# Kernel tuning notes

Measured on AMD Instinct MI355X. Metric: run time of the kernel, lower is better.

Reference implementation:

```python
import jax, jax.numpy as jnp
import numpy as np

B, S, H, NH, L, MLP_MULT = 4, 1024, 1024, 16, 2, 4
DK = H // NH
EPS = 1e-5


def setup_inputs() -> dict:
    key = jax.random.key(0)
    ks = jax.random.split(key, 8)
    p = lambda k, shape: jax.random.normal(k, shape, dtype=jnp.float32) * 0.02
    return {
        'hidden_states': jax.random.normal(ks[0], (B, S, H), dtype=jnp.float32),
        'attn_w': p(ks[1], (L, H, 3 * H)),
        'attn_b': jnp.zeros((L, 3 * H), jnp.float32),
        'proj_w': p(ks[2], (L, H, H)),
        'proj_b': jnp.zeros((L, H), jnp.float32),
        'fc_w': p(ks[3], (L, H, MLP_MULT * H)),
        'fc_b': jnp.zeros((L, MLP_MULT * H), jnp.float32),
        'fc2_w': p(ks[4], (L, MLP_MULT * H, H)),
        'fc2_b': jnp.zeros((L, H), jnp.float32),
        'ln1_g': jnp.ones((L, H), jnp.float32),
        'ln1_b': jnp.zeros((L, H), jnp.float32),
        'ln2_g': jnp.ones((L, H), jnp.float32),
        'ln2_b': jnp.zeros((L, H), jnp.float32),
        'position_ids': jnp.arange(S, dtype=jnp.int32),
    }


def _ln(x, g, b):
    m = jnp.mean(x, axis=-1, keepdims=True)
    v = jnp.var(x, axis=-1, keepdims=True)
    return (x - m) * jax.lax.rsqrt(v + EPS) * g + b


def _rotate_half(x):
    x1, x2 = jnp.split(x, 2, axis=-1)
    return jnp.concatenate((-x2, x1), axis=-1)


def _forward(hidden_states, attn_w, attn_b, proj_w, proj_b, fc_w, fc_b,
             fc2_w, fc2_b, ln1_g, ln1_b, ln2_g, ln2_b, position_ids):
    # rotary tables (fp32 math, as in RotaryEmbedding.forward)
    inv_freq = 1.0 / (10000.0 ** (jnp.arange(0, DK, 2, dtype=jnp.float32) / DK))
    freqs = position_ids.astype(jnp.float32)[:, None] * inv_freq[None, :]  # [S, DK/2]
    emb = jnp.concatenate((freqs, freqs), axis=-1)                          # [S, DK]
    cos = jnp.cos(emb)[None, None]  # [1,1,S,DK]
    sin = jnp.sin(emb)[None, None]
    causal = jnp.tril(jnp.ones((S, S), dtype=bool))
    neg = jnp.finfo(jnp.float32).min
    scale = 1.0 / np.sqrt(DK).astype(np.float32)

    h = hidden_states
    for i in range(L):
        # attention block
        x = _ln(h, ln1_g[i], ln1_b[i])
        qkv = x @ attn_w[i] + attn_b[i]                  # Conv1D c_attn
        q, k, v = jnp.split(qkv, 3, axis=-1)
        heads = lambda t: t.reshape(B, S, NH, DK).transpose(0, 2, 1, 3)
        q, k, v = heads(q), heads(k), heads(v)           # [B,NH,S,DK]
        q = q * cos + _rotate_half(q) * sin
        k = k * cos + _rotate_half(k) * sin
        # fp32 QK^T (baddbmm with alpha=scale, beta=0)
        w = jnp.einsum('bhqd,bhkd->bhqk', q.astype(jnp.float32),
                       k.astype(jnp.float32)) * scale    # [B,NH,S,S]
        w = jnp.where(causal, w, neg)
        w = jax.nn.softmax(w, axis=-1).astype(v.dtype)   # attn dropout is identity (eval)
        a = jnp.einsum('bhqk,bhkd->bhqd', w, v)
        a = a.transpose(0, 2, 1, 3).reshape(B, S, H)     # merge_heads
        h = h + (a @ proj_w[i] + proj_b[i])              # c_proj + residual
        # MLP block (gelu_new == tanh-approx gelu)
        x = _ln(h, ln2_g[i], ln2_b[i])
        mid = jax.nn.gelu(x @ fc_w[i] + fc_b[i], approximate=True)
        h = h + (mid @ fc2_w[i] + fc2_b[i])
    return h


def reference(hidden_states, attn_w, attn_b, proj_w, proj_b, fc_w, fc_b,
              fc2_w, fc2_b, ln1_g, ln1_b, ln2_g, ln2_b, position_ids):
    return _forward(hidden_states, attn_w, attn_b, proj_w, proj_b, fc_w, fc_b,
                    fc2_w, fc2_b, ln1_g, ln1_b, ln2_g, ln2_b, position_ids)
```

## Files before the change

### kernel.cpp

```cpp
#include <hip/hip_runtime.h>

#define B_ 4
#define S_ 1024
#define H_ 1024
#define NH_ 16
#define DK_ 64
#define MLPH_ 4096
#define EPS_ 1e-5f

typedef __attribute__((ext_vector_type(8))) short short8_t;
typedef __attribute__((ext_vector_type(8))) unsigned short ushort8_t;
typedef __attribute__((ext_vector_type(4))) float f32x4;

__device__ __forceinline__ unsigned short f2bf(float f) {
  unsigned int u = __float_as_uint(f);
  u = u + 0x7fffu + ((u >> 16) & 1u);
  return (unsigned short)(u >> 16);
}
__device__ __forceinline__ float bf2f(unsigned short b) {
  return __uint_as_float(((unsigned int)b) << 16);
}

__device__ __forceinline__ void gload16(const void* g, void* l) {
  typedef const __attribute__((address_space(1))) unsigned int GU;
  typedef __attribute__((address_space(3))) unsigned int LU;
  __builtin_amdgcn_global_load_lds((GU*)(size_t)g, (LU*)(unsigned int)(size_t)l, 16, 0, 0);
}

__device__ __forceinline__ float gelu_tanh(float x) {
  float y = 1.5957691216057308f * (x + 0.044715f * x * x * x);
  return x / (1.0f + __expf(-y));
}

__global__ __launch_bounds__(256) void wconv(const float* __restrict__ src,
                                             unsigned short* __restrict__ dst,
                                             int K, int N) {
  __shared__ float t[32][33];
  int n0 = blockIdx.x * 32, k0 = blockIdx.y * 32;
  int tid = threadIdx.x;
  int r = tid >> 3, c = (tid & 7) * 4;
  const float* s = src + (size_t)(k0 + r) * N + n0 + c;
  float4 v = *(const float4*)s;
  t[r][c] = v.x; t[r][c + 1] = v.y; t[r][c + 2] = v.z; t[r][c + 3] = v.w;
  __syncthreads();
  ushort4 o;
  o.x = f2bf(t[c + 0][r]); o.y = f2bf(t[c + 1][r]);
  o.z = f2bf(t[c + 2][r]); o.w = f2bf(t[c + 3][r]);
  *(ushort4*)(dst + (size_t)(n0 + r) * K + k0 + c) = o;
}

__global__ __launch_bounds__(256) void ln_kernel(const float* __restrict__ x,
                                                 const float* __restrict__ g,
                                                 const float* __restrict__ b,
                                                 unsigned short* __restrict__ y) {
  int row = blockIdx.x, tid = threadIdx.x;
  const float* xp = x + (size_t)row * H_;
  float4 v = *((const float4*)xp + tid);
  float s  = v.x + v.y + v.z + v.w;
  float s2 = v.x * v.x + v.y * v.y + v.z * v.z + v.w * v.w;
  #pragma unroll
  for (int o = 1; o < 64; o <<= 1) {
    s  += __shfl_xor(s, o, 64);
    s2 += __shfl_xor(s2, o, 64);
  }
  __shared__ float r1[4], r2[4];
  if ((tid & 63) == 0) { r1[tid >> 6] = s; r2[tid >> 6] = s2; }
  __syncthreads();
  s  = r1[0] + r1[1] + r1[2] + r1[3];
  s2 = r2[0] + r2[1] + r2[2] + r2[3];
  float mean = s * (1.0f / H_);
  float var  = s2 * (1.0f / H_) - mean * mean;
  float inv  = rsqrtf(var + EPS_);
  float4 gv = *((const float4*)g + tid);
  float4 bv = *((const float4*)b + tid);
  ushort4 o;
  o.x = f2bf((v.x - mean) * inv * gv.x + bv.x);
  o.y = f2bf((v.y - mean) * inv * gv.y + bv.y);
  o.z = f2bf((v.z - mean) * inv * gv.z + bv.z);
  o.w = f2bf((v.w - mean) * inv * gv.w + bv.w);
  *(ushort4*)(y + (size_t)row * H_ + tid * 4) = o;
}

__global__ __launch_bounds__(256) void rope_bf(unsigned short* qkv, const int* __restrict__ pos) {
  int idx = blockIdx.x * 256 + threadIdx.x;
  int d = idx & 31;
  int hh = (idx >> 5) & 15;
  int s = (idx >> 9) & 1023;
  int b = idx >> 19;
  size_t base = ((size_t)(b * S_ + s)) * 3072 + hh * 64;
  float inv = __expf(-9.210340371976184f * ((float)d * 0.03125f));
  float th = (float)pos[s] * inv;
  float cs = cosf(th), sn = sinf(th);
  unsigned short* qp = qkv + base;
  unsigned short* kp = qkv + base + 1024;
  float q0 = bf2f(qp[d]), q1 = bf2f(qp[d + 32]);
  float k0 = bf2f(kp[d]), k1 = bf2f(kp[d + 32]);
  qp[d]      = f2bf(q0 * cs - q1 * sn);
  qp[d + 32] = f2bf(q1 * cs + q0 * sn);
  kp[d]      = f2bf(k0 * cs - k1 * sn);
  kp[d + 32] = f2bf(k1 * cs + k0 * sn);
}

template <int MODE, int NT>
__global__ __launch_bounds__(256) void gemm_mfma(
    const unsigned short* __restrict__ A, const unsigned short* __restrict__ Bt,
    const float* __restrict__ bias, const float* __restrict__ resid,
    void* __restrict__ outp, int M, int N, int K) {
  constexpr int BN = NT * 32;
  constexpr int CB = BN / 32;
  __shared__ __align__(16) unsigned short As[2][128 * 64];
  __shared__ __align__(16) unsigned short Bs[2][BN * 64];
  int tid = threadIdx.x;
  int w = tid >> 6, lane = tid & 63;
  int gx = gridDim.x;
  int nwg = gx * gridDim.y;
  int bid = blockIdx.y * gx + blockIdx.x;
  int cpx = nwg >> 3;
  int swz = (bid & 7) * cpx + (bid >> 3);
  int m0 = (swz / gx) * 128, n0 = (swz % gx) * BN;
  int wr = w >> 1, wc = w & 1;
  int fr = lane & 15, kg = lane >> 4;
  f32x4 acc[4][NT];
  #pragma unroll
  for (int m = 0; m < 4; m++)
    #pragma unroll
    for (int n = 0; n < NT; n++) {
      acc[m][n][0] = 0.f; acc[m][n][1] = 0.f; acc[m][n][2] = 0.f; acc[m][n][3] = 0.f;
    }
  int srow = lane >> 3;
  int scol = ((lane & 7) ^ srow) * 8;
  const unsigned short* Ap = A  + (size_t)(m0 + w * 32 + srow) * K + scol;
  const unsigned short* Bp = Bt + (size_t)(n0 + w * (8 * CB) + srow) * K + scol;
  int sx = (fr & 7);
  int nk = K >> 6;
  {
    char* AsB = (char*)As[0] + w * 4096;
    char* BsB = (char*)Bs[0] + w * CB * 1024;
    #pragma unroll
    for (int i = 0; i < 4; i++) gload16(Ap + (size_t)i * 8 * K, AsB + i * 1024);
    #pragma unroll
    for (int i = 0; i < CB; i++) gload16(Bp + (size_t)i * 8 * K, BsB + i * 1024);
  }
  __syncthreads();
  for (int t = 0; t < nk; t++) {
    int cur = t & 1;
    if (t + 1 < nk) {
      const unsigned short* Ap2 = Ap + (size_t)(t + 1) * 64;
      const unsigned short* Bp2 = Bp + (size_t)(t + 1) * 64;
      char* AsB = (char*)As[cur ^ 1] + w * 4096;
      char* BsB = (char*)Bs[cur ^ 1] + w * CB * 1024;
      #pragma unroll
      for (int i = 0; i < 4; i++) gload16(Ap2 + (size_t)i * 8 * K, AsB + i * 1024);
      #pragma unroll
      for (int i = 0; i < CB; i++) gload16(Bp2 + (size_t)i * 8 * K, BsB + i * 1024);
    }
    #pragma unroll
    for (int kk = 0; kk < 2; kk++) {
      int slot = ((kk * 4 + kg) ^ sx) << 4;
      short8_t af[4], bfr[NT];
      #pragma unroll
      for (int m = 0; m < 4; m++)
        af[m] = *(const short8_t*)((char*)As[cur] + (wr * 64 + m * 16 + fr) * 128 + slot);
      #pragma unroll
      for (int n = 0; n < NT; n++)
        bfr[n] = *(const short8_t*)((char*)Bs[cur] + (wc * (NT * 16) + n * 16 + fr) * 128 + slot);
      #pragma unroll
      for (int m = 0; m < 4; m++)
        #pragma unroll
        for (int n = 0; n < NT; n++)
          acc[m][n] = __builtin_amdgcn_mfma_f32_16x16x32_bf16(af[m], bfr[n], acc[m][n], 0, 0, 0);
    }
    __syncthreads();
  }
  #pragma unroll
  for (int n = 0; n < NT; n++) {
    int col = n0 + wc * (NT * 16) + n * 16 + fr;
    float bv = bias[col];
    #pragma unroll
    for (int m = 0; m < 4; m++) {
      int row = m0 + wr * 64 + m * 16 + kg * 4;
      #pragma unroll
      for (int r = 0; r < 4; r++) {
        float v = acc[m][n][r] + bv;
        size_t idx = (size_t)(row + r) * N + col;
        if (MODE == 2)      ((float*)outp)[idx] = resid[idx] + v;
        else if (MODE == 1) ((unsigned short*)outp)[idx] = f2bf(gelu_tanh(v));
        else                ((unsigned short*)outp)[idx] = f2bf(v);
      }
    }
  }
}

__global__ __launch_bounds__(256) void attn5(const unsigned short* __restrict__ qkv,
                                             unsigned short* __restrict__ aout) {
  __shared__ __align__(16) unsigned short Ks[2][64 * 64];
  __shared__ __align__(16) unsigned short Vt[2][64 * 64];
  __shared__ __align__(16) unsigned short Ps[4][2][16 * 64];
  int tid = threadIdx.x;
  int w = tid >> 6, lane = tid & 63;
  int fr = lane & 15, kg = lane >> 4;
  int qt = (int)gridDim.x - 1 - (int)blockIdx.x;
  int q0 = qt * 128;
  int head = blockIdx.y, b = blockIdx.z;
  const unsigned short* base = qkv + ((size_t)b * S_) * 3072 + head * 64;

  short8_t qa0[2], qa1[2];
  #pragma unroll
  for (int g = 0; g < 2; g++) {
    const unsigned short* qp = base + (size_t)(q0 + w * 32 + g * 16 + fr) * 3072 + kg * 8;
    qa0[g] = *(const short8_t*)qp;
    qa1[g] = *(const short8_t*)(qp + 32);
  }

  f32x4 acc[2][4];
  float mrun[2][4], lrun[2][4];
  #pragma unroll
  for (int g = 0; g < 2; g++)
    #pragma unroll
    for (int n = 0; n < 4; n++) {
      acc[g][n][0] = 0.f; acc[g][n][1] = 0.f; acc[g][n][2] = 0.f; acc[g][n][3] = 0.f;
      mrun[g][n] = -3.0e38f; lrun[g][n] = 0.f;
    }

  int skv = lane;
  int sd0 = w * 16;

  const unsigned short* kp0 = base + 1024 + (size_t)skv * 3072 + sd0;
  short8_t ka = *(const short8_t*)kp0;
  short8_t kb = *(const short8_t*)(kp0 + 8);
  short8_t va = *(const short8_t*)(kp0 + 1024);
  short8_t vb = *(const short8_t*)(kp0 + 1032);

  int ntiles = 2 * qt + 2;
  for (int t = 0; t < ntiles; t++) {
    int cur = t & 1;
    {
      unsigned kbyte = skv * 128 + sd0 * 2;
      unsigned ksw = (skv & 7) << 4;
      *(short8_t*)((char*)Ks[cur] + (kbyte ^ ksw)) = ka;
      *(short8_t*)((char*)Ks[cur] + ((kbyte + 16) ^ ksw)) = kb;
      #pragma unroll
      for (int j = 0; j < 8; j++) {
        int d0 = sd0 + j, d1 = sd0 + 8 + j;
        *(unsigned short*)((char*)Vt[cur] + ((d0 * 128 + skv * 2) ^ ((d0 & 7) << 4))) = (unsigned short)va[j];
        *(unsigned short*)((char*)Vt[cur] + ((d1 * 128 + skv * 2) ^ ((d1 & 7) << 4))) = (unsigned short)vb[j];
      }
    }
    if (t + 1 < ntiles) {
      const unsigned short* kp = base + 1024 + (size_t)((t + 1) * 64 + skv) * 3072 + sd0;
      ka = *(const short8_t*)kp;
      kb = *(const short8_t*)(kp + 8);
      va = *(const short8_t*)(kp + 1024);
      vb = *(const short8_t*)(kp + 1032);
    }
    __syncthreads();
    f32x4 s[2][4];
    {
      short8_t b0[4], b1[4];
      #pragma unroll
      for (int n = 0; n < 4; n++) {
        int kvrow = n * 16 + fr;
        unsigned sw = (kvrow & 7) << 4;
        b0[n] = *(const short8_t*)((char*)Ks[cur] + ((kvrow * 128 + kg * 16) ^ sw));
        b1[n] = *(const short8_t*)((char*)Ks[cur] + ((kvrow * 128 + 64 + kg * 16) ^ sw));
      }
      __builtin_amdgcn_s_setprio(1);
      #pragma unroll
      for (int g = 0; g < 2; g++)
        #pragma unroll
        for (int n = 0; n < 4; n++) {
          f32x4 z; z[0] = 0.f; z[1] = 0.f; z[2] = 0.f; z[3] = 0.f;
          z = __builtin_amdgcn_mfma_f32_16x16x32_bf16(qa0[g], b0[n], z, 0, 0, 0);
          z = __builtin_amdgcn_mfma_f32_16x16x32_bf16(qa1[g], b1[n], z, 0, 0, 0);
          s[g][n] = z;
        }
      __builtin_amdgcn_s_setprio(0);
    }
    bool diag = (t >= 2 * qt);
    float pmax[2][4];
    #pragma unroll
    for (int g = 0; g < 2; g++)
      #pragma unroll
      for (int r = 0; r < 4; r++) {
        int qrow = q0 + w * 32 + g * 16 + kg * 4 + r;
        float rm = -3.0e38f;
        #pragma unroll
        for (int n = 0; n < 4; n++) {
          float sv = s[g][n][r] * 0.125f;
          if (diag && (t * 64 + n * 16 + fr > qrow)) sv = -3.0e38f;
          s[g][n][r] = sv;
          rm = fmaxf(rm, sv);
        }
        pmax[g][r] = rm;
      }
    bool need = false;
    #pragma unroll
    for (int g = 0; g < 2; g++)
      #pragma unroll
      for (int r = 0; r < 4; r++) need |= (pmax[g][r] > mrun[g][r] + 8.f);
    if (__any(need)) {
      #pragma unroll
      for (int g = 0; g < 2; g++)
        #pragma unroll
        for (int r = 0; r < 4; r++) {
          float rm = pmax[g][r];
          rm = fmaxf(rm, __shfl_xor(rm, 1, 64));
          rm = fmaxf(rm, __shfl_xor(rm, 2, 64));
          rm = fmaxf(rm, __shfl_xor(rm, 4, 64));
          rm = fmaxf(rm, __shfl_xor(rm, 8, 64));
          float mn = fmaxf(mrun[g][r], rm);
          float sc = __expf(mrun[g][r] - mn);
          mrun[g][r] = mn;
          lrun[g][r] *= sc;
          #pragma unroll
          for (int n = 0; n < 4; n++) acc[g][n][r] *= sc;
        }
    }
    #pragma unroll
    for (int g = 0; g < 2; g++)
      #pragma unroll
      for (int r = 0; r < 4; r++) {
        float ls = 0.f;
        int row = kg * 4 + r;
        #pragma unroll
        for (int n = 0; n < 4; n++) {
          float e = __expf(s[g][n][r] - mrun[g][r]);
          ls += e;
          int col = n * 16 + fr;
          *(unsigned short*)((char*)Ps[w][g] + ((row * 128 + col * 2) ^ ((row & 7) << 4))) = f2bf(e);
        }
        lrun[g][r] += ls;
      }
    asm volatile("s_waitcnt lgkmcnt(0)" ::: "memory");
    unsigned psw = (fr & 7) << 4;
    short8_t pa0[2], pa1[2];
    #pragma unroll
    for (int g = 0; g < 2; g++) {
      pa0[g] = *(const short8_t*)((char*)Ps[w][g] + ((fr * 128 + kg * 16) ^ psw));
      pa1[g] = *(const short8_t*)((char*)Ps[w][g] + ((fr * 128 + 64 + kg * 16) ^ psw));
    }
    __builtin_amdgcn_s_setprio(1);
    #pragma unroll
    for (int n = 0; n < 4; n++) {
      int d = n * 16 + fr;
      unsigned sw = (d & 7) << 4;
      short8_t v0 = *(const short8_t*)((char*)Vt[cur] + ((d * 128 + kg * 16) ^ sw));
      short8_t v1 = *(const short8_t*)((char*)Vt[cur] + ((d * 128 + 64 + kg * 16) ^ sw));
      #pragma unroll
      for (int g = 0; g < 2; g++) {
        acc[g][n] = __builtin_amdgcn_mfma_f32_16x16x32_bf16(pa0[g], v0, acc[g][n], 0, 0, 0);
        acc[g][n] = __builtin_amdgcn_mfma_f32_16x16x32_bf16(pa1[g], v1, acc[g][n], 0, 0, 0);
      }
    }
    __builtin_amdgcn_s_setprio(0);
  }
  #pragma unroll
  for (int g = 0; g < 2; g++)
    #pragma unroll
    for (int r = 0; r < 4; r++) {
      float ls = lrun[g][r];
      ls += __shfl_xor(ls, 1, 64);
      ls += __shfl_xor(ls, 2, 64);
      ls += __shfl_xor(ls, 4, 64);
      ls += __shfl_xor(ls, 8, 64);
      float inv = 1.0f / ls;
      size_t row = (size_t)b * S_ + q0 + w * 32 + g * 16 + kg * 4 + r;
      unsigned short* op = aout + row * H_ + head * 64 + fr;
      #pragma unroll
      for (int n = 0; n < 4; n++) op[n * 16] = f2bf(acc[g][n][r] * inv);
    }
}

extern "C" void kernel_launch(void* const* d_in, const int* in_sizes, int n_in,
                              void* d_out, int out_size, void* d_ws, size_t ws_size,
                              hipStream_t stream) {
  const float* hs     = (const float*)d_in[0];
  const float* attn_w = (const float*)d_in[1];
  const float* attn_b = (const float*)d_in[2];
  const float* proj_w = (const float*)d_in[3];
  const float* proj_b = (const float*)d_in[4];
  const float* fc_w   = (const float*)d_in[5];
  const float* fc_b   = (const float*)d_in[6];
  const float* fc2_w  = (const float*)d_in[7];
  const float* fc2_b  = (const float*)d_in[8];
  const float* ln1_g  = (const float*)d_in[9];
  const float* ln1_b  = (const float*)d_in[10];
  const float* ln2_g  = (const float*)d_in[11];
  const float* ln2_b  = (const float*)d_in[12];
  const int*   pos    = (const int*)d_in[13];

  float* hres = (float*)d_out;
  const size_t rows = (size_t)B_ * S_;

  unsigned short* wQ    = (unsigned short*)d_ws;
  unsigned short* wP    = wQ  + (size_t)2 * 3072 * 1024;
  unsigned short* wF1   = wP  + (size_t)2 * 1024 * 1024;
  unsigned short* wF2   = wF1 + (size_t)2 * 4096 * 1024;
  unsigned short* xbf   = wF2 + (size_t)2 * 1024 * 4096;
  unsigned short* qkvbf = xbf + rows * H_;
  unsigned short* midbf = qkvbf + rows * 3 * H_;
  unsigned short* aoutbf= midbf + rows * MLPH_;

  hipMemcpyAsync(hres, hs, rows * H_ * sizeof(float), hipMemcpyDeviceToDevice, stream);

  for (int l = 0; l < 2; l++) {
    wconv<<<dim3(96, 32), 256, 0, stream>>>(attn_w + (size_t)l * 1024 * 3072,
                                            wQ + (size_t)l * 3072 * 1024, 1024, 3072);
    wconv<<<dim3(32, 32), 256, 0, stream>>>(proj_w + (size_t)l * 1024 * 1024,
                                            wP + (size_t)l * 1024 * 1024, 1024, 1024);
    wconv<<<dim3(128, 32), 256, 0, stream>>>(fc_w + (size_t)l * 1024 * 4096,
                                             wF1 + (size_t)l * 4096 * 1024, 1024, 4096);
    wconv<<<dim3(32, 128), 256, 0, stream>>>(fc2_w + (size_t)l * 4096 * 1024,
                                             wF2 + (size_t)l * 1024 * 4096, 4096, 1024);
  }

  for (int l = 0; l < 2; l++) {
    ln_kernel<<<rows, 256, 0, stream>>>(hres, ln1_g + l * H_, ln1_b + l * H_, xbf);
    gemm_mfma<0, 4><<<dim3(24, 32), 256, 0, stream>>>(
        xbf, wQ + (size_t)l * 3072 * 1024, attn_b + (size_t)l * 3072, nullptr,
        qkvbf, 4096, 3072, 1024);
    rope_bf<<<8192, 256, 0, stream>>>(qkvbf, pos);
    attn5<<<dim3(8, 16, 4), 256, 0, stream>>>(qkvbf, aoutbf);
    gemm_mfma<2, 2><<<dim3(16, 32), 256, 0, stream>>>(
        aoutbf, wP + (size_t)l * 1024 * 1024, proj_b + (size_t)l * 1024, hres,
        hres, 4096, 1024, 1024);
    ln_kernel<<<rows, 256, 0, stream>>>(hres, ln2_g + l * H_, ln2_b + l * H_, xbf);
    gemm_mfma<1, 4><<<dim3(32, 32), 256, 0, stream>>>(
        xbf, wF1 + (size_t)l * 4096 * 1024, fc_b + (size_t)l * 4096, nullptr,
        midbf, 4096, 4096, 1024);
    gemm_mfma<2, 2><<<dim3(16, 32), 256, 0, stream>>>(
        midbf, wF2 + (size_t)l * 1024 * 4096, fc2_b + (size_t)l * 1024, hres,
        hres, 4096, 1024, 4096);
  }
}
```

Measured before the change: 466.2 us.

## Fuse RoPE into QKV GEMM epilogue, transpose attention MFMA layout, batch weight conversion

The separate rope_bf kernel is removed and rotary embedding is applied in a new MODE 3 epilogue of the QKV GEMM, using the fact that each 128-column tile holds both halves of a head. The attention kernel now computes S^T and O^T by swapping the MFMA operands, so each lane owns one query row: softmax max and sum reductions need only two shuffles, exp2 replaces exp with a pre-folded log2e scale, P is packed with v_cvt_pk_bf16_f32, and output stores are vectorized. Weight-conversion launches are merged across layers with a z grid dimension. This removes a full read-modify-write pass over Q and K and cuts per-row reduction work, at the cost of more epilogue complexity and sincos inside the GEMM.

```diff
diff --git a/kernel.cpp b/kernel.cpp
--- a/kernel.cpp
+++ b/kernel.cpp
@@ -32,10 +32,12 @@
   return x / (1.0f + __expf(-y));
 }
 
-__global__ __launch_bounds__(256) void wconv(const float* __restrict__ src,
-                                             unsigned short* __restrict__ dst,
+__global__ __launch_bounds__(256) void wconv(const float* __restrict__ src0,
+                                             unsigned short* __restrict__ dst0,
                                              int K, int N) {
   __shared__ float t[32][33];
+  const float* src = src0 + (size_t)blockIdx.z * K * N;
+  unsigned short* dst = dst0 + (size_t)blockIdx.z * N * K;
   int n0 = blockIdx.x * 32, k0 = blockIdx.y * 32;
   int tid = threadIdx.x;
   int r = tid >> 3, c = (tid & 7) * 4;
@@ -81,31 +83,11 @@
   *(ushort4*)(y + (size_t)row * H_ + tid * 4) = o;
 }
 
-__global__ __launch_bounds__(256) void rope_bf(unsigned short* qkv, const int* __restrict__ pos) {
-  int idx = blockIdx.x * 256 + threadIdx.x;
-  int d = idx & 31;
-  int hh = (idx >> 5) & 15;
-  int s = (idx >> 9) & 1023;
-  int b = idx >> 19;
-  size_t base = ((size_t)(b * S_ + s)) * 3072 + hh * 64;
-  float inv = __expf(-9.210340371976184f * ((float)d * 0.03125f));
-  float th = (float)pos[s] * inv;
-  float cs = cosf(th), sn = sinf(th);
-  unsigned short* qp = qkv + base;
-  unsigned short* kp = qkv + base + 1024;
-  float q0 = bf2f(qp[d]), q1 = bf2f(qp[d + 32]);
-  float k0 = bf2f(kp[d]), k1 = bf2f(kp[d + 32]);
-  qp[d]      = f2bf(q0 * cs - q1 * sn);
-  qp[d + 32] = f2bf(q1 * cs + q0 * sn);
-  kp[d]      = f2bf(k0 * cs - k1 * sn);
-  kp[d + 32] = f2bf(k1 * cs + k0 * sn);
-}
-
 template <int MODE, int NT>
 __global__ __launch_bounds__(256) void gemm_mfma(
     const unsigned short* __restrict__ A, const unsigned short* __restrict__ Bt,
     const float* __restrict__ bias, const float* __restrict__ resid,
-    void* __restrict__ outp, int M, int N, int K) {
+    void* __restrict__ outp, int M, int N, int K, const int* __restrict__ pos) {
   constexpr int BN = NT * 32;
   constexpr int CB = BN / 32;
   __shared__ __align__(16) unsigned short As[2][128 * 64];
@@ -172,6 +154,48 @@
     }
     __syncthreads();
   }
+  if (MODE == 3) {
+    int seg = n0 >> 10;
+    if (seg < 2) {
+      #pragma unroll
+      for (int n = 0; n < 2; n++) {
+        int col0 = n0 + wc * 64 + n * 16 + fr;
+        int d2 = n * 16 + fr;
+        float invf = __expf(-0.2878231366242557f * (float)d2);
+        float bv0 = bias[col0], bv2 = bias[col0 + 32];
+        #pragma unroll
+        for (int m = 0; m < 4; m++) {
+          int row = m0 + wr * 64 + m * 16 + kg * 4;
+          #pragma unroll
+          for (int r = 0; r < 4; r++) {
+            int s = (row + r) & (S_ - 1);
+            float th = (float)pos[s] * invf;
+            float sn, cs;
+            __sincosf(th, &sn, &cs);
+            float a0 = acc[m][n][r] + bv0;
+            float a2 = acc[m][n + 2][r] + bv2;
+            size_t base = (size_t)(row + r) * N;
+            ((unsigned short*)outp)[base + col0]      = f2bf(a0 * cs - a2 * sn);
+            ((unsigned short*)outp)[base + col0 + 32] = f2bf(a2 * cs + a0 * sn);
+          }
+        }
+      }
+    } else {
+      #pragma unroll
+      for (int n = 0; n < NT; n++) {
+        int col = n0 + wc * (NT * 16) + n * 16 + fr;
+        float bv = bias[col];
+        #pragma unroll
+        for (int m = 0; m < 4; m++) {
+          int row = m0 + wr * 64 + m * 16 + kg * 4;
+          #pragma unroll
+          for (int r = 0; r < 4; r++)
+            ((unsigned short*)outp)[(size_t)(row + r) * N + col] = f2bf(acc[m][n][r] + bv);
+        }
+      }
+    }
+    return;
+  }
   #pragma unroll
   for (int n = 0; n < NT; n++) {
     int col = n0 + wc * (NT * 16) + n * 16 + fr;
@@ -191,11 +215,13 @@
   }
 }
 
-__global__ __launch_bounds__(256) void attn5(const unsigned short* __restrict__ qkv,
+__global__ __launch_bounds__(256) void attn6(const unsigned short* __restrict__ qkv,
                                              unsigned short* __restrict__ aout) {
   __shared__ __align__(16) unsigned short Ks[2][64 * 64];
   __shared__ __align__(16) unsigned short Vt[2][64 * 64];
   __shared__ __align__(16) unsigned short Ps[4][2][16 * 64];
+  const float SCL2 = 0.18033688011112443f;
+  const float THR2 = 11.541560327111708f;
   int tid = threadIdx.x;
   int w = tid >> 6, lane = tid & 63;
   int fr = lane & 15, kg = lane >> 4;
@@ -213,17 +239,21 @@
   }
 
   f32x4 acc[2][4];
-  float mrun[2][4], lrun[2][4];
-  #pragma unroll
-  for (int g = 0; g < 2; g++)
+  float mrun[2], lrun[2];
+  #pragma unroll
+  for (int g = 0; g < 2; g++) {
+    mrun[g] = -3.0e38f; lrun[g] = 0.f;
     #pragma unroll
     for (int n = 0; n < 4; n++) {
       acc[g][n][0] = 0.f; acc[g][n][1] = 0.f; acc[g][n][2] = 0.f; acc[g][n][3] = 0.f;
-      mrun[g][n] = -3.0e38f; lrun[g][n] = 0.f;
-    }
+    }
+  }
 
   int skv = lane;
   int sd0 = w * 16;
+  int qg[2];
+  qg[0] = q0 + w * 32 + fr;
+  qg[1] = qg[0] + 16;
 
   const unsigned short* kp0 = base + 1024 + (size_t)skv * 3072 + sd0;
   short8_t ka = *(const short8_t*)kp0;
@@ -254,7 +284,7 @@
       vb = *(const short8_t*)(kp + 1032);
     }
     __syncthreads();
-    f32x4 s[2][4];
+    f32x4 st[2][4];
     {
       short8_t b0[4], b1[4];
       #pragma unroll
@@ -270,67 +300,63 @@
         #pragma unroll
         for (int n = 0; n < 4; n++) {
           f32x4 z; z[0] = 0.f; z[1] = 0.f; z[2] = 0.f; z[3] = 0.f;
-          z = __builtin_amdgcn_mfma_f32_16x16x32_bf16(qa0[g], b0[n], z, 0, 0, 0);
-          z = __builtin_amdgcn_mfma_f32_16x16x32_bf16(qa1[g], b1[n], z, 0, 0, 0);
-          s[g][n] = z;
+          z = __builtin_amdgcn_mfma_f32_16x16x32_bf16(b0[n], qa0[g], z, 0, 0, 0);
+          z = __builtin_amdgcn_mfma_f32_16x16x32_bf16(b1[n], qa1[g], z, 0, 0, 0);
+          st[g][n] = z;
         }
       __builtin_amdgcn_s_setprio(0);
     }
     bool diag = (t >= 2 * qt);
-    float pmax[2][4];
-    #pragma unroll
-    for (int g = 0; g < 2; g++)
-      #pragma unroll
-      for (int r = 0; r < 4; r++) {
-        int qrow = q0 + w * 32 + g * 16 + kg * 4 + r;
-        float rm = -3.0e38f;
-        #pragma unroll
-        for (int n = 0; n < 4; n++) {
-          float sv = s[g][n][r] * 0.125f;
-          if (diag && (t * 64 + n * 16 + fr > qrow)) sv = -3.0e38f;
-          s[g][n][r] = sv;
+    float pmax[2];
+    #pragma unroll
+    for (int g = 0; g < 2; g++) {
+      float rm = -3.0e38f;
+      #pragma unroll
+      for (int n = 0; n < 4; n++)
+        #pragma unroll
+        for (int j = 0; j < 4; j++) {
+          float sv = st[g][n][j] * SCL2;
+          if (diag && (t * 64 + n * 16 + kg * 4 + j > qg[g])) sv = -1.0e30f;
+          st[g][n][j] = sv;
           rm = fmaxf(rm, sv);
         }
-        pmax[g][r] = rm;
-      }
-    bool need = false;
-    #pragma unroll
-    for (int g = 0; g < 2; g++)
-      #pragma unroll
-      for (int r = 0; r < 4; r++) need |= (pmax[g][r] > mrun[g][r] + 8.f);
+      pmax[g] = rm;
+    }
+    bool need = (pmax[0] > mrun[0] + THR2) | (pmax[1] > mrun[1] + THR2);
     if (__any(need)) {
       #pragma unroll
-      for (int g = 0; g < 2; g++)
-        #pragma unroll
-        for (int r = 0; r < 4; r++) {
-          float rm = pmax[g][r];
-          rm = fmaxf(rm, __shfl_xor(rm, 1, 64));
-          rm = fmaxf(rm, __shfl_xor(rm, 2, 64));
-          rm = fmaxf(rm, __shfl_xor(rm, 4, 64));
-          rm = fmaxf(rm, __shfl_xor(rm, 8, 64));
-          float mn = fmaxf(mrun[g][r], rm);
-          float sc = __expf(mrun[g][r] - mn);
-          mrun[g][r] = mn;
-          lrun[g][r] *= sc;
-          #pragma unroll
-          for (int n = 0; n < 4; n++) acc[g][n][r] *= sc;
+      for (int g = 0; g < 2; g++) {
+        float rm = pmax[g];
+        rm = fmaxf(rm, __shfl_xor(rm, 16, 64));
+        rm = fmaxf(rm, __shfl_xor(rm, 32, 64));
+        float mn = fmaxf(mrun[g], rm);
+        float sc = exp2f(mrun[g] - mn);
+        mrun[g] = mn;
+        lrun[g] *= sc;
+        #pragma unroll
+        for (int n = 0; n < 4; n++) {
+          acc[g][n][0] *= sc; acc[g][n][1] *= sc; acc[g][n][2] *= sc; acc[g][n][3] *= sc;
         }
-    }
-    #pragma unroll
-    for (int g = 0; g < 2; g++)
-      #pragma unroll
-      for (int r = 0; r < 4; r++) {
-        float ls = 0.f;
-        int row = kg * 4 + r;
-        #pragma unroll
-        for (int n = 0; n < 4; n++) {
-          float e = __expf(s[g][n][r] - mrun[g][r]);
-          ls += e;
-          int col = n * 16 + fr;
-          *(unsigned short*)((char*)Ps[w][g] + ((row * 128 + col * 2) ^ ((row & 7) << 4))) = f2bf(e);
-        }
-        lrun[g][r] += ls;
-      }
+      }
+    }
+    #pragma unroll
+    for (int g = 0; g < 2; g++) {
+      float ls = 0.f;
+      #pragma unroll
+      for (int n = 0; n < 4; n++) {
+        float e0 = exp2f(st[g][n][0] - mrun[g]);
+        float e1 = exp2f(st[g][n][1] - mrun[g]);
+        float e2 = exp2f(st[g][n][2] - mrun[g]);
+        float e3 = exp2f(st[g][n][3] - mrun[g]);
+        ls += (e0 + e1) + (e2 + e3);
+        unsigned lo, hi;
+        asm("v_cvt_pk_bf16_f32 %0, %1, %2" : "=v"(lo) : "v"(e0), "v"(e1));
+        asm("v_cvt_pk_bf16_f32 %0, %1, %2" : "=v"(hi) : "v"(e2), "v"(e3));
+        uint2 pk; pk.x = lo; pk.y = hi;
+        *(uint2*)((char*)Ps[w][g] + ((fr * 128 + n * 32 + kg * 8) ^ ((fr & 7) << 4))) = pk;
+      }
+      lrun[g] += ls;
+    }
     asm volatile("s_waitcnt lgkmcnt(0)" ::: "memory");
     unsigned psw = (fr & 7) << 4;
     short8_t pa0[2], pa1[2];
@@ -348,27 +374,30 @@
       short8_t v1 = *(const short8_t*)((char*)Vt[cur] + ((d * 128 + 64 + kg * 16) ^ sw));
       #pragma unroll
       for (int g = 0; g < 2; g++) {
-        acc[g][n] = __builtin_amdgcn_mfma_f32_16x16x32_bf16(pa0[g], v0, acc[g][n], 0, 0, 0);
-        acc[g][n] = __builtin_amdgcn_mfma_f32_16x16x32_bf16(pa1[g], v1, acc[g][n], 0, 0, 0);
+        acc[g][n] = __builtin_amdgcn_mfma_f32_16x16x32_bf16(v0, pa0[g], acc[g][n], 0, 0, 0);
+        acc[g][n] = __builtin_amdgcn_mfma_f32_16x16x32_bf16(v1, pa1[g], acc[g][n], 0, 0, 0);
       }
     }
     __builtin_amdgcn_s_setprio(0);
   }
   #pragma unroll
-  for (int g = 0; g < 2; g++)
-    #pragma unroll
-    for (int r = 0; r < 4; r++) {
-      float ls = lrun[g][r];
-      ls += __shfl_xor(ls, 1, 64);
-      ls += __shfl_xor(ls, 2, 64);
-      ls += __shfl_xor(ls, 4, 64);
-      ls += __shfl_xor(ls, 8, 64);
-      float inv = 1.0f / ls;
-      size_t row = (size_t)b * S_ + q0 + w * 32 + g * 16 + kg * 4 + r;
-      unsigned short* op = aout + row * H_ + head * 64 + fr;
-      #pragma unroll
-      for (int n = 0; n < 4; n++) op[n * 16] = f2bf(acc[g][n][r] * inv);
-    }
+  for (int g = 0; g < 2; g++) {
+    float ls = lrun[g];
+    ls += __shfl_xor(ls, 16, 64);
+    ls += __shfl_xor(ls, 32, 64);
+    float inv = 1.0f / ls;
+    size_t row = (size_t)b * S_ + q0 + w * 32 + g * 16 + fr;
+    unsigned short* op = aout + row * H_ + head * 64 + kg * 4;
+    #pragma unroll
+    for (int n = 0; n < 4; n++) {
+      ushort4 o;
+      o.x = f2bf(acc[g][n][0] * inv);
+      o.y = f2bf(acc[g][n][1] * inv);
+      o.z = f2bf(acc[g][n][2] * inv);
+      o.w = f2bf(acc[g][n][3] * inv);
+      *(ushort4*)(op + n * 16) = o;
+    }
+  }
 }
 
 extern "C" void kernel_launch(void* const* d_in, const int* in_sizes, int n_in,
@@ -403,33 +432,26 @@
 
   hipMemcpyAsync(hres, hs, rows * H_ * sizeof(float), hipMemcpyDeviceToDevice, stream);
 
-  for (int l = 0; l < 2; l++) {
-    wconv<<<dim3(96, 32), 256, 0, stream>>>(attn_w + (size_t)l * 1024 * 3072,
-                                            wQ + (size_t)l * 3072 * 1024, 1024, 3072);
-    wconv<<<dim3(32, 32), 256, 0, stream>>>(proj_w + (size_t)l * 1024 * 1024,
-                                            wP + (size_t)l * 1024 * 1024, 1024, 1024);
-    wconv<<<dim3(128, 32), 256, 0, stream>>>(fc_w + (size_t)l * 1024 * 4096,
-                                             wF1 + (size_t)l * 4096 * 1024, 1024, 4096);
-    wconv<<<dim3(32, 128), 256, 0, stream>>>(fc2_w + (size_t)l * 4096 * 1024,
-                                             wF2 + (size_t)l * 1024 * 4096, 4096, 1024);
-  }
+  wconv<<<dim3(96, 32, 2), 256, 0, stream>>>(attn_w, wQ, 1024, 3072);
+  wconv<<<dim3(32, 32, 2), 256, 0, stream>>>(proj_w, wP, 1024, 1024);
+  wconv<<<dim3(128, 32, 2), 256, 0, stream>>>(fc_w, wF1, 1024, 4096);
+  wconv<<<dim3(32, 128, 2), 256, 0, stream>>>(fc2_w, wF2, 4096, 1024);
 
   for (int l = 0; l < 2; l++) {
     ln_kernel<<<rows, 256, 0, stream>>>(hres, ln1_g + l * H_, ln1_b + l * H_, xbf);
-    gemm_mfma<0, 4><<<dim3(24, 32), 256, 0, stream>>>(
+    gemm_mfma<3, 4><<<dim3(24, 32), 256, 0, stream>>>(
         xbf, wQ + (size_t)l * 3072 * 1024, attn_b + (size_t)l * 3072, nullptr,
-        qkvbf, 4096, 3072, 1024);
-    rope_bf<<<8192, 256, 0, stream>>>(qkvbf, pos);
-    attn5<<<dim3(8, 16, 4), 256, 0, stream>>>(qkvbf, aoutbf);
+        qkvbf, 4096, 3072, 1024, pos);
+    attn6<<<dim3(8, 16, 4), 256, 0, stream>>>(qkvbf, aoutbf);
     gemm_mfma<2, 2><<<dim3(16, 32), 256, 0, stream>>>(
         aoutbf, wP + (size_t)l * 1024 * 1024, proj_b + (size_t)l * 1024, hres,
-        hres, 4096, 1024, 1024);
+        hres, 4096, 1024, 1024, nullptr);
     ln_kernel<<<rows, 256, 0, stream>>>(hres, ln2_g + l * H_, ln2_b + l * H_, xbf);
     gemm_mfma<1, 4><<<dim3(32, 32), 256, 0, stream>>>(
         xbf, wF1 + (size_t)l * 4096 * 1024, fc_b + (size_t)l * 4096, nullptr,
-        midbf, 4096, 4096, 1024);
+        midbf, 4096, 4096, 1024, nullptr);
     gemm_mfma<2, 2><<<dim3(16, 32), 256, 0, stream>>>(
         midbf, wF2 + (size_t)l * 1024 * 4096, fc2_b + (size_t)l * 1024, hres,
-        hres, 4096, 1024, 4096);
-  }
-}
+        hres, 4096, 1024, 4096, nullptr);
+  }
+}
```

Result: faster. 447.7 us (-4.0%).
